# Kernel tuning notes

Hardware: AMD Instinct MI355X
Metric: run time of the kernel (lower is better)

Reference implementation:

```python
import jax, jax.numpy as jnp
import numpy as np

# model dims (see init_kwargs)
HID = 2048
H = 16
Q_LORA = 768
KV_LORA = 512
QK_NOPE = 128
QK_ROPE = 64
QK_HEAD = QK_NOPE + QK_ROPE  # 192
V_DIM = 128
HI = 8        # indexer heads
DI = 128      # indexer head dim
TOPK = 512    # index_topk
EPS = 1e-5
B, S = 1, 2048


def rms_norm(x, w):
    return x * jax.lax.rsqrt(jnp.mean(x * x, -1, keepdims=True) + EPS) * w


def layer_norm(x, w, b):
    m = jnp.mean(x, -1, keepdims=True)
    v = jnp.mean((x - m) ** 2, -1, keepdims=True)
    return (x - m) * jax.lax.rsqrt(v + EPS) * w + b


def rotate_half(x):
    x1, x2 = jnp.split(x, 2, axis=-1)
    return jnp.concatenate([-x2, x1], axis=-1)


def rope_bshd(x, cos, sin):
    # x: [B,S,H,D], cos/sin: [B,S,D] -> broadcast over heads (unsqueeze_dim=2)
    return x * cos[:, :, None, :] + rotate_half(x) * sin[:, :, None, :]


def setup_inputs() -> dict:
    key = jax.random.key(0)
    ks = jax.random.split(key, 16)
    std = 0.02
    hidden_states = jax.random.normal(ks[0], (B, S, HID), jnp.float32)
    # real RoPE tables, theta=10000, head_dim=QK_ROPE
    inv_freq = 1.0 / (10000.0 ** (np.arange(0, QK_ROPE, 2, dtype=np.float32) / QK_ROPE))
    freqs = np.arange(S, dtype=np.float32)[:, None] * inv_freq[None, :]  # [S, ROPE/2]
    emb = np.concatenate([freqs, freqs], axis=-1)
    cos = jnp.asarray(np.cos(emb))[None]  # [1,S,ROPE]
    sin = jnp.asarray(np.sin(emb))[None]
    w = lambda k, shp: jax.random.normal(k, shp, jnp.float32) * std
    return {
        'hidden_states': hidden_states, 'cos': cos, 'sin': sin,
        'wq_a': w(ks[1], (Q_LORA, HID)),
        'q_a_norm_w': jnp.ones((Q_LORA,), jnp.float32),
        'wq_b': w(ks[2], (H * QK_HEAD, Q_LORA)),
        'wkv_a': w(ks[3], (KV_LORA + QK_ROPE, HID)),
        'kv_a_norm_w': jnp.ones((KV_LORA,), jnp.float32),
        'wkv_b': w(ks[4], (H * (QK_NOPE + V_DIM), KV_LORA)),
        'wo': w(ks[5], (HID, H * V_DIM)),
        'idx_wq_b': w(ks[6], (HI * DI, Q_LORA)),
        'idx_wk': w(ks[7], (DI, HID)),
        'idx_k_norm_w': jnp.ones((DI,), jnp.float32),
        'idx_k_norm_b': jnp.zeros((DI,), jnp.float32),
        'idx_weights_w': w(ks[8], (HI, HID)),
    }


def reference(hidden_states, cos, sin, wq_a, q_a_norm_w, wq_b, wkv_a, kv_a_norm_w,
              wkv_b, wo, idx_wq_b, idx_wk, idx_k_norm_w, idx_k_norm_b, idx_weights_w):
    b, s, _ = hidden_states.shape
    # ---- MLA projections ----
    q_lora = rms_norm(hidden_states @ wq_a.T, q_a_norm_w)              # [B,S,Q_LORA]
    q = (q_lora @ wq_b.T).reshape(b, s, H, QK_HEAD)
    q_nope, q_rope = jnp.split(q, [QK_NOPE], axis=-1)
    q_rope = rope_bshd(q_rope, cos, sin)

    kv = hidden_states @ wkv_a.T                                        # [B,S,KV_LORA+ROPE]
    kv_lat, k_rope = jnp.split(kv, [KV_LORA], axis=-1)
    k_rope = k_rope * cos + rotate_half(k_rope) * sin                   # shared MQA rope key [B,S,ROPE]
    kv_lat = rms_norm(kv_lat, kv_a_norm_w)
    kvb = (kv_lat @ wkv_b.T).reshape(b, s, H, QK_NOPE + V_DIM)
    k_nope, value = jnp.split(kvb, [QK_NOPE], axis=-1)

    queries = jnp.concatenate([q_nope, q_rope], axis=-1)                # [B,S,H,QK_HEAD]
    keys = jnp.concatenate(
        [k_nope, jnp.broadcast_to(k_rope[:, :, None, :], (b, s, H, QK_ROPE))], axis=-1)

    # ---- lightning indexer (DSA): per-query top-k KV selection ----
    iq = (q_lora @ idx_wq_b.T).reshape(b, s, HI, DI)
    iq_rot, iq_pass = jnp.split(iq, [QK_ROPE], axis=-1)
    iq = jnp.concatenate([rope_bshd(iq_rot, cos, sin), iq_pass], axis=-1)
    ik = layer_norm(hidden_states @ idx_wk.T, idx_k_norm_w, idx_k_norm_b)  # [B,S,DI]
    ik_rot, ik_pass = jnp.split(ik, [QK_ROPE], axis=-1)
    ik = jnp.concatenate([ik_rot * cos + rotate_half(ik_rot) * sin, ik_pass], axis=-1)

    iscores = jnp.einsum('bqhd,bkd->bqhk', iq, ik) * (DI ** -0.5)       # [B,S,HI,S]
    iw = (hidden_states @ idx_weights_w.T) * (HI ** -0.5)               # [B,S,HI]
    iscore = jnp.einsum('bqh,bqhk->bqk', iw, iscores)                   # [B,S,S]

    causal = jnp.tril(jnp.ones((s, s), bool))
    iscore = jnp.where(causal[None], iscore, -1e9)
    _, topk_idx = jax.lax.top_k(iscore, TOPK)                           # [B,S,TOPK]
    allow = jnp.zeros((b, s, s), bool).at[
        jnp.arange(b)[:, None, None], jnp.arange(s)[None, :, None], topk_idx].set(True)
    allow = allow & causal[None]                                        # topk AND causal

    # ---- masked attention ----
    scale = QK_HEAD ** -0.5
    scores = jnp.einsum('bqhd,bkhd->bhqk', queries, keys) * scale       # [B,H,S,S]
    scores = jnp.where(allow[:, None], scores, -jnp.inf)
    probs = jax.nn.softmax(scores, axis=-1)
    out = jnp.einsum('bhqk,bkhd->bqhd', probs, value).reshape(b, s, H * V_DIM)
    return out @ wo.T
```

## Files before the change

### kernel.cpp

```cpp
#include <hip/hip_runtime.h>
#include <hip/hip_bf16.h>
#include <stdint.h>
#include <math.h>

#define S_LEN 2048
#define HIDDEN 2048
#define NHEAD 16
#define QLORA 768
#define KVLORA 512
#define QKNOPE 128
#define QKROPE 64
#define QKHEAD 192
#define VDIM 128
#define HIN 8
#define DIN 128
#define TOPKN 512
#define EPSF 1e-5f
#define DLAT 576
#define SCALE_ATT 0.07216878364870322f

typedef __bf16 bf16x8 __attribute__((ext_vector_type(8)));
typedef float  f32x4  __attribute__((ext_vector_type(4)));

static __device__ __forceinline__ float wave_reduce_sum(float v) {
    #pragma unroll
    for (int off = 32; off > 0; off >>= 1) v += __shfl_down(v, off);
    return v;
}

static __device__ __forceinline__ void splitw(__bf16* __restrict__ H,
                                              __bf16* __restrict__ L,
                                              size_t idx, float v) {
    __bf16 h = (__bf16)v;
    H[idx] = h;
    L[idx] = (__bf16)(v - (float)h);
}

static __device__ __forceinline__ void gll16(const __bf16* g, __bf16* lds_base) {
    __builtin_amdgcn_global_load_lds(
        (const __attribute__((address_space(1))) uint32_t*)g,
        (__attribute__((address_space(3))) uint32_t*)lds_base, 16, 0, 0);
}

#define PREP_BLOCKS 17280
__global__ __launch_bounds__(256) void prep_all(
        const float* __restrict__ hid,     __bf16* hidH,  __bf16* hidL,
        const float* __restrict__ wq_a,    __bf16* wqaH,  __bf16* wqaL,
        const float* __restrict__ idx_wq_b,__bf16* iwqH,  __bf16* iwqL,
        const float* __restrict__ idx_wk,  __bf16* iwkH,  __bf16* iwkL,
        const float* __restrict__ wq_b,    __bf16* wq_b_bf,
        const float* __restrict__ wkv_a,   __bf16* wkv_a_bf,
        const float* __restrict__ wkv_b,   __bf16* wkv_b_bf,
        const float* __restrict__ wo,      __bf16* wo_bf,
        __bf16* wknt) {
    int b = blockIdx.x, tid = threadIdx.x;
    const float* src; __bf16 *dH = nullptr, *dL = nullptr, *dC = nullptr;
    int base;
    if (b < 4096)        { src = hid;      dH = hidH; dL = hidL; base = b; }
    else if (b < 5632)   { src = wq_a;     dH = wqaH; dL = wqaL; base = b - 4096; }
    else if (b < 6400)   { src = idx_wq_b; dH = iwqH; dL = iwqL; base = b - 5632; }
    else if (b < 6656)   { src = idx_wk;   dH = iwkH; dL = iwkL; base = b - 6400; }
    else if (b < 8960)   { src = wq_b;     dC = wq_b_bf;  base = b - 6656; }
    else if (b < 10112)  { src = wkv_a;    dC = wkv_a_bf; base = b - 8960; }
    else if (b < 12160)  { src = wkv_b;    dC = wkv_b_bf; base = b - 10112; }
    else if (b < 16256)  { src = wo;       dC = wo_bf;    base = b - 12160; }
    else {
        int e = ((b - 16256) * 256 + tid) * 4;
        int c = e & 511, d = (e >> 9) & 127, h = e >> 16;
        f32x4 v = *(const f32x4*)(wkv_b + ((size_t)(h * 256 + d)) * 512 + c);
        #pragma unroll
        for (int j = 0; j < 4; ++j)
            wknt[(size_t)h * 65536 + (c + j) * 128 + d] = (__bf16)v[j];
        return;
    }
    int i = (base * 256 + tid) * 4;
    f32x4 v = *(const f32x4*)(src + i);
    if (dC) {
        #pragma unroll
        for (int j = 0; j < 4; ++j) dC[i + j] = (__bf16)v[j];
    } else {
        #pragma unroll
        for (int j = 0; j < 4; ++j) splitw(dH, dL, i + j, v[j]);
    }
}

#define GBM 128
#define GBN 64
#define GBK 32
template <typename OutT>
static __device__ __forceinline__ void gemm_s_core(
        const __bf16* __restrict__ A, const __bf16* __restrict__ B,
        OutT* __restrict__ C, int K, int lda, int ldb, int ldc,
        int bx, int by) {
    __shared__ __bf16 sAs[GBM * GBK];
    __shared__ __bf16 sBs[GBN * GBK];
    int tid = threadIdx.x;
    int lane = tid & 63, wid = tid >> 6;
    int quad = lane >> 4, l16 = lane & 15;
    int wm = wid >> 1, wn = wid & 1;
    int row0 = by * GBM, col0 = bx * GBN;
    int lr = lane >> 2, lk = (lane & 3) * 8;

    f32x4 acc[4][2] = {};

    for (int k0 = 0; k0 < K; k0 += GBK) {
        #pragma unroll
        for (int c = 0; c < 2; ++c) {
            int rb = (wid * 2 + c) * 16;
            gll16(A + (size_t)(row0 + rb + lr) * lda + k0 + lk, sAs + rb * GBK);
        }
        gll16(B + (size_t)(col0 + wid * 16 + lr) * ldb + k0 + lk, sBs + wid * 16 * GBK);
        __syncthreads();
        bf16x8 af[4], bfr[2];
        #pragma unroll
        for (int mi = 0; mi < 4; ++mi)
            af[mi] = *(const bf16x8*)&sAs[(wm * 64 + mi * 16 + l16) * GBK + quad * 8];
        #pragma unroll
        for (int ni = 0; ni < 2; ++ni)
            bfr[ni] = *(const bf16x8*)&sBs[(wn * 32 + ni * 16 + l16) * GBK + quad * 8];
        #pragma unroll
        for (int mi = 0; mi < 4; ++mi)
            #pragma unroll
            for (int ni = 0; ni < 2; ++ni)
                acc[mi][ni] = __builtin_amdgcn_mfma_f32_16x16x32_bf16(
                    af[mi], bfr[ni], acc[mi][ni], 0, 0, 0);
        __syncthreads();
    }
    #pragma unroll
    for (int mi = 0; mi < 4; ++mi)
        #pragma unroll
        for (int ni = 0; ni < 2; ++ni)
            #pragma unroll
            for (int r = 0; r < 4; ++r) {
                int row = row0 + wm * 64 + mi * 16 + quad * 4 + r;
                int col = col0 + wn * 32 + ni * 16 + l16;
                C[(size_t)row * ldc + col] = (OutT)acc[mi][ni][r];
            }
}

template <typename OutT>
__global__ __launch_bounds__(256) void gemm_s(const __bf16* __restrict__ A,
                                              const __bf16* __restrict__ B,
                                              OutT* __restrict__ C,
                                              int K, int lda, int ldb, int ldc,
                                              long sA, long sB, long sC) {
    gemm_s_core<OutT>(A + (size_t)blockIdx.z * sA, B + (size_t)blockIdx.z * sB,
                      C + (size_t)blockIdx.z * sC, K, lda, ldb, ldc,
                      blockIdx.x, blockIdx.y);
}

template <bool CAUSAL>
static __device__ __forceinline__ void gemm3_core(
        const __bf16* __restrict__ Ah, const __bf16* __restrict__ Al,
        const __bf16* __restrict__ Bh, const __bf16* __restrict__ Bl,
        float* __restrict__ C, int K, int lda, int ldb, int ldc,
        int row_base, int bx, int by) {
    int row0 = by * GBM + row_base, col0 = bx * GBN;
    if (CAUSAL && col0 > row0 + GBM - 1) return;
    __shared__ __bf16 sAh[GBM * GBK], sAl[GBM * GBK];
    __shared__ __bf16 sBh[GBN * GBK], sBl[GBN * GBK];
    int tid = threadIdx.x;
    int lane = tid & 63, wid = tid >> 6;
    int quad = lane >> 4, l16 = lane & 15;
    int wm = wid >> 1, wn = wid & 1;
    int lr = lane >> 2, lk = (lane & 3) * 8;

    f32x4 acc[4][2] = {};

    for (int k0 = 0; k0 < K; k0 += GBK) {
        #pragma unroll
        for (int c = 0; c < 2; ++c) {
            int rb = (wid * 2 + c) * 16;
            size_t go = (size_t)(row0 + rb + lr) * lda + k0 + lk;
            gll16(Ah + go, sAh + rb * GBK);
            gll16(Al + go, sAl + rb * GBK);
        }
        {
            size_t go = (size_t)(col0 + wid * 16 + lr) * ldb + k0 + lk;
            gll16(Bh + go, sBh + wid * 16 * GBK);
            gll16(Bl + go, sBl + wid * 16 * GBK);
        }
        __syncthreads();
        bf16x8 afh[4], afl[4], bfh[2], bfl[2];
        #pragma unroll
        for (int mi = 0; mi < 4; ++mi) {
            int o = (wm * 64 + mi * 16 + l16) * GBK + quad * 8;
            afh[mi] = *(const bf16x8*)&sAh[o];
            afl[mi] = *(const bf16x8*)&sAl[o];
        }
        #pragma unroll
        for (int ni = 0; ni < 2; ++ni) {
            int o = (wn * 32 + ni * 16 + l16) * GBK + quad * 8;
            bfh[ni] = *(const bf16x8*)&sBh[o];
            bfl[ni] = *(const bf16x8*)&sBl[o];
        }
        #pragma unroll
        for (int mi = 0; mi < 4; ++mi)
            #pragma unroll
            for (int ni = 0; ni < 2; ++ni) {
                acc[mi][ni] = __builtin_amdgcn_mfma_f32_16x16x32_bf16(
                    afl[mi], bfh[ni], acc[mi][ni], 0, 0, 0);
                acc[mi][ni] = __builtin_amdgcn_mfma_f32_16x16x32_bf16(
                    afh[mi], bfl[ni], acc[mi][ni], 0, 0, 0);
                acc[mi][ni] = __builtin_amdgcn_mfma_f32_16x16x32_bf16(
                    afh[mi], bfh[ni], acc[mi][ni], 0, 0, 0);
            }
        __syncthreads();
    }
    #pragma unroll
    for (int mi = 0; mi < 4; ++mi)
        #pragma unroll
        for (int ni = 0; ni < 2; ++ni)
            #pragma unroll
            for (int r = 0; r < 4; ++r) {
                int row = row0 + wm * 64 + mi * 16 + quad * 4 + r;
                int col = col0 + wn * 32 + ni * 16 + l16;
                C[(size_t)row * ldc + col] = acc[mi][ni][r];
            }
}

__global__ __launch_bounds__(256) void gemm3_ks(const __bf16* __restrict__ Ah,
                                                const __bf16* __restrict__ Al,
                                                const __bf16* __restrict__ Bh,
                                                const __bf16* __restrict__ Bl,
                                                float* __restrict__ Cpart,
                                                int Ksub, int lda, int ldb, int ldc,
                                                long sC) {
    int bz = blockIdx.z, koff = bz * Ksub;
    gemm3_core<false>(Ah + koff, Al + koff, Bh + koff, Bl + koff,
                      Cpart + (size_t)bz * sC, Ksub, lda, ldb, ldc, 0,
                      blockIdx.x, blockIdx.y);
}

__global__ __launch_bounds__(256) void fused_mid(
        const __bf16* __restrict__ qlH, const __bf16* __restrict__ qlL,
        const __bf16* __restrict__ wq_b_bf, __bf16* __restrict__ qbuf_bf,
        const __bf16* __restrict__ hidH, const __bf16* __restrict__ hidL,
        const __bf16* __restrict__ wkv_a_bf, float* __restrict__ kv,
        const __bf16* __restrict__ iwqH, const __bf16* __restrict__ iwqL,
        float* __restrict__ iqraw,
        const __bf16* __restrict__ iwkH, const __bf16* __restrict__ iwkL,
        float* __restrict__ ikraw) {
    int b = blockIdx.x;
    if (b < 768) {
        gemm_s_core<__bf16>(qlH, wq_b_bf, qbuf_bf, QLORA, QLORA, QLORA,
                            NHEAD * QKHEAD, b % 48, b / 48);
    } else if (b < 912) {
        int r = b - 768;
        gemm_s_core<float>(hidH, wkv_a_bf, kv, HIDDEN, HIDDEN, HIDDEN, DLAT,
                           r % 9, r / 9);
    } else if (b < 1168) {
        int r = b - 912;
        gemm3_core<false>(qlH, qlL, iwqH, iwqL, iqraw, QLORA, QLORA, QLORA,
                          HIN * DIN, 0, r & 15, r >> 4);
    } else {
        int r = b - 1168;
        gemm3_core<false>(hidH, hidL, iwkH, iwkL, ikraw, HIDDEN, HIDDEN, HIDDEN,
                          DIN, 0, r & 1, r >> 1);
    }
}

__global__ __launch_bounds__(256) void fused2(
        const __bf16* __restrict__ qbuf_bf, const __bf16* __restrict__ wknt,
        __bf16* __restrict__ qeff,
        const __bf16* __restrict__ cqH, const __bf16* __restrict__ cqL,
        const __bf16* __restrict__ ikH, const __bf16* __restrict__ ikL,
        float* __restrict__ iscore) {
    int b = blockIdx.x;
    if (b < 2048) {
        int bx = b & 7, by = (b >> 3) & 15, bz = b >> 7;
        gemm_s_core<__bf16>(qbuf_bf + bz * QKHEAD, wknt + (size_t)bz * 512 * 128,
                            qeff + bz * DLAT, 128, NHEAD * QKHEAD, 128,
                            NHEAD * DLAT, bx, by);
    } else {
        int r = b - 2048;
        gemm3_core<true>(cqH, cqL, ikH, ikL, iscore, DIN, DIN, DIN, S_LEN,
                         TOPKN, r & 31, r >> 5);
    }
}

__global__ __launch_bounds__(256) void rmsnorm_split4(const float* __restrict__ p,
                                                      long ps,
                                                      const float* __restrict__ w,
                                                      __bf16* __restrict__ yH,
                                                      __bf16* __restrict__ yL, int ncols) {
    int row = blockIdx.x, tid = threadIdx.x;
    const float* p0 = p + (size_t)row * ncols;
    float ss = 0.f;
    for (int c = tid; c < ncols; c += 256) {
        float v = p0[c] + p0[ps + c] + p0[2 * ps + c] + p0[3 * ps + c];
        ss += v * v;
    }
    __shared__ float red[4];
    ss = wave_reduce_sum(ss);
    if ((tid & 63) == 0) red[tid >> 6] = ss;
    __syncthreads();
    float tot = red[0] + red[1] + red[2] + red[3];
    float inv = rsqrtf(tot / (float)ncols + EPSF);
    for (int c = tid; c < ncols; c += 256) {
        float v = p0[c] + p0[ps + c] + p0[2 * ps + c] + p0[3 * ps + c];
        splitw(yH, yL, (size_t)row * ncols + c, v * inv * w[c]);
    }
}

__global__ __launch_bounds__(256) void fused_post(
        const __bf16* __restrict__ qbuf, __bf16* __restrict__ qeff,
        const float* __restrict__ kv, const float* __restrict__ kvw,
        __bf16* __restrict__ klat,
        const float* __restrict__ ikraw, const float* __restrict__ lnw,
        const float* __restrict__ lnb, __bf16* __restrict__ ikH, __bf16* __restrict__ ikL,
        const float* __restrict__ iqraw, const float* __restrict__ hid,
        const float* __restrict__ iww, __bf16* __restrict__ cqH, __bf16* __restrict__ cqL,
        const float* __restrict__ cosT, const float* __restrict__ sinT) {
    int s = blockIdx.x, tid = threadIdx.x;
    int lane = tid & 63, wid = tid >> 6;

    for (int i = tid; i < NHEAD * 32; i += 256) {
        int h = i >> 5, d = i & 31;
        const __bf16* base = qbuf + (size_t)s * (NHEAD * QKHEAD) + h * QKHEAD + QKNOPE;
        float x1 = (float)base[d], x2 = (float)base[d + 32];
        float c1 = cosT[s * 64 + d],      s1 = sinT[s * 64 + d];
        float c2 = cosT[s * 64 + d + 32], s2 = sinT[s * 64 + d + 32];
        __bf16* o = qeff + (size_t)s * (NHEAD * DLAT) + h * DLAT + 512;
        o[d]      = (__bf16)(x1 * c1 - x2 * s1);
        o[d + 32] = (__bf16)(x2 * c2 + x1 * s2);
    }

    {
        const float* row = kv + (size_t)s * DLAT;
        float ss = 0.f;
        for (int c = tid; c < KVLORA; c += 256) { float v = row[c]; ss += v * v; }
        __shared__ float redB[4];
        ss = wave_reduce_sum(ss);
        if (lane == 0) redB[wid] = ss;
        __syncthreads();
        float tot = redB[0] + redB[1] + redB[2] + redB[3];
        float inv = rsqrtf(tot / (float)KVLORA + EPSF);
        __bf16* orow = klat + (size_t)s * DLAT;
        for (int c = tid; c < KVLORA; c += 256)
            orow[c] = (__bf16)(row[c] * inv * kvw[c]);
        if (tid < 32) {
            int d = tid;
            float x1 = row[KVLORA + d], x2 = row[KVLORA + d + 32];
            float c1 = cosT[s * 64 + d],      s1 = sinT[s * 64 + d];
            float c2 = cosT[s * 64 + d + 32], s2 = sinT[s * 64 + d + 32];
            orow[512 + d]      = (__bf16)(x1 * c1 - x2 * s1);
            orow[512 + d + 32] = (__bf16)(x2 * c2 + x1 * s2);
        }
    }

    {
        float x = (tid < DIN) ? ikraw[(size_t)s * DIN + tid] : 0.f;
        __shared__ float redC1[4], redC2[4], sy[DIN];
        float sm = wave_reduce_sum(x);
        if (lane == 0) redC1[wid] = sm;
        __syncthreads();
        float mean = (redC1[0] + redC1[1] + redC1[2] + redC1[3]) / (float)DIN;
        float dx = (tid < DIN) ? (x - mean) : 0.f;
        float vs = wave_reduce_sum(dx * dx);
        if (lane == 0) redC2[wid] = vs;
        __syncthreads();
        float var = (redC2[0] + redC2[1] + redC2[2] + redC2[3]) / (float)DIN;
        if (tid < DIN) sy[tid] = dx * rsqrtf(var + EPSF) * lnw[tid] + lnb[tid];
        __syncthreads();
        size_t ro = (size_t)s * DIN;
        if (tid < 32) {
            int d = tid;
            float c1 = cosT[s * 64 + d],      s1 = sinT[s * 64 + d];
            float c2 = cosT[s * 64 + d + 32], s2 = sinT[s * 64 + d + 32];
            splitw(ikH, ikL, ro + d,      sy[d] * c1 - sy[d + 32] * s1);
            splitw(ikH, ikL, ro + d + 32, sy[d + 32] * c2 + sy[d] * s2);
        } else if (tid >= 64 && tid < DIN) {
            splitw(ikH, ikL, ro + tid, sy[tid]);
        }
        __syncthreads();
    }

    {
        __shared__ float redD[4][HIN], siw[HIN];
        float a8[HIN] = {};
        const float* xr = hid + (size_t)s * HIDDEN;
        for (int c = tid; c < HIDDEN; c += 256) {
            float x = xr[c];
            #pragma unroll
            for (int h = 0; h < HIN; ++h) a8[h] += x * iww[h * HIDDEN + c];
        }
        #pragma unroll
        for (int h = 0; h < HIN; ++h) a8[h] = wave_reduce_sum(a8[h]);
        if (lane == 0)
            #pragma unroll
            for (int h = 0; h < HIN; ++h) redD[wid][h] = a8[h];
        __syncthreads();
        if (tid < HIN)
            siw[tid] = redD[0][tid] + redD[1][tid] + redD[2][tid] + redD[3][tid];
        __syncthreads();
        if (tid < DIN) {
            int d = tid;
            float acc = 0.f;
            float c1 = 0.f, s1 = 0.f;
            if (d < 64) { c1 = cosT[s * 64 + d]; s1 = sinT[s * 64 + d]; }
            #pragma unroll
            for (int h = 0; h < HIN; ++h) {
                const float* base = iqraw + ((size_t)s * HIN + h) * DIN;
                float v;
                if (d < 32)       v = base[d] * c1 - base[d + 32] * s1;
                else if (d < 64)  v = base[d] * c1 + base[d - 32] * s1;
                else              v = base[d];
                acc += siw[h] * v;
            }
            splitw(cqH, cqL, (size_t)s * DIN + d, acc * 0.03125f);
        }
    }
}

__global__ __launch_bounds__(256) void topk_rows(const float* __restrict__ iscore,
                                                 int* __restrict__ topk) {
    int q = TOPKN + blockIdx.x;
    int n = q + 1;
    __shared__ uint32_t skey[S_LEN];
    __shared__ int hist[256];
    __shared__ int scan[256];
    __shared__ uint32_t sp;
    __shared__ int sr, pos;
    int tid = threadIdx.x;
    const float* row = iscore + (size_t)q * S_LEN;
    for (int i = tid; i < n; i += 256) {
        uint32_t u = __float_as_uint(row[i]);
        skey[i] = (u & 0x80000000u) ? ~u : (u | 0x80000000u);
    }
    __syncthreads();
    uint32_t prefix = 0;
    int remk = TOPKN;
    for (int pass = 0; pass < 4; ++pass) {
        int shift = 24 - 8 * pass;
        uint32_t pmask = pass ? (0xFFFFFFFFu << (shift + 8)) : 0u;
        hist[tid] = 0;
        __syncthreads();
        for (int i = tid; i < n; i += 256) {
            uint32_t u = skey[i];
            if ((u & pmask) == prefix) atomicAdd(&hist[(u >> shift) & 255], 1);
        }
        __syncthreads();
        scan[tid] = hist[tid];
        __syncthreads();
        for (int step = 1; step < 256; step <<= 1) {
            int v = (tid + step < 256) ? scan[tid + step] : 0;
            __syncthreads();
            scan[tid] += v;
            __syncthreads();
        }
        int Sb = scan[tid];
        int Snext = (tid < 255) ? scan[tid + 1] : 0;
        if (Sb >= remk && Snext < remk) {
            sp = prefix | ((uint32_t)tid << shift);
            sr = remk - Snext;
        }
        __syncthreads();
        prefix = sp; remk = sr;
        __syncthreads();
    }
    if (tid == 0) pos = 0;
    __syncthreads();
    int* orow = topk + (size_t)q * TOPKN;
    for (int i = tid; i < n; i += 256) {
        if (skey[i] > prefix) { int p = atomicAdd(&pos, 1); orow[p] = i; }
    }
    __syncthreads();
    int base = pos;
    int chunk = (n + 255) >> 8;
    int lo = tid * chunk, hiEnd = lo + chunk;
    if (hiEnd > n) hiEnd = n;
    int cnt = 0;
    for (int i = lo; i < hiEnd; ++i) cnt += (skey[i] == prefix);
    scan[tid] = cnt;
    __syncthreads();
    for (int step = 1; step < 256; step <<= 1) {
        int v = (tid >= step) ? scan[tid - step] : 0;
        __syncthreads();
        scan[tid] += v;
        __syncthreads();
    }
    int r = scan[tid] - cnt;
    for (int i = lo; i < hiEnd && r < remk; ++i) {
        if (skey[i] == prefix) { orow[base + r] = i; ++r; }
    }
}

#define SKS 584
__global__ __launch_bounds__(256) void attn2(const __bf16* __restrict__ qeff,
                                             const __bf16* __restrict__ klat,
                                             const int* __restrict__ topk,
                                             __bf16* __restrict__ o_lat) {
    int q = (blockIdx.x * 997) & (S_LEN - 1);
    int tid = threadIdx.x;
    int lane = tid & 63, wid = tid >> 6;
    int l16 = lane & 15, quad = lane >> 4;
    int wn = wid & 1, wk = wid >> 1;

    __shared__ short sK[32 * SKS];
    __shared__ float s_part[2][16][37];
    __shared__ float s_S[16][38];
    __shared__ float s_m[16], s_l[16], s_alpha[16], s_inv[16];

    int L = (q < TOPKN) ? (q + 1) : TOPKN;
    int nt = (L + 31) >> 5;
    const int* idxr = topk + (size_t)q * TOPKN;

    bf16x8 qf[9];
    const __bf16* qrow = qeff + (size_t)q * (NHEAD * DLAT) + l16 * DLAT + wk * 288 + quad * 8;
    #pragma unroll
    for (int s = 0; s < 9; ++s) qf[s] = *(const bf16x8*)(qrow + s * 32);

    if (tid < 16) { s_m[tid] = -1e30f; s_l[tid] = 0.f; }

    f32x4 oacc[8];
    #pragma unroll
    for (int i = 0; i < 8; ++i) oacc[i] = (f32x4){0.f, 0.f, 0.f, 0.f};

    int srow = tid >> 3, schk = tid & 7;

    for (int t = 0; t < nt; ++t) {
        int ki = t * 32 + srow;
        int gk = 0;
        if (ki < L) gk = (q < TOPKN) ? ki : idxr[ki];
        const uint4* src = (const uint4*)(klat + (size_t)gk * DLAT) + schk * 9;
        uint4* dst = (uint4*)((char*)sK + srow * (SKS * 2) + schk * 144);
        #pragma unroll
        for (int c = 0; c < 9; ++c) dst[c] = src[c];
        __syncthreads();

        f32x4 sacc = {0.f, 0.f, 0.f, 0.f};
        const short* kbase = sK + (wn * 16 + l16) * SKS + wk * 288 + quad * 8;
        #pragma unroll
        for (int s = 0; s < 9; ++s) {
            bf16x8 kf = *(const bf16x8*)(kbase + s * 32);
            sacc = __builtin_amdgcn_mfma_f32_16x16x32_bf16(qf[s], kf, sacc, 0, 0, 0);
        }
        #pragma unroll
        for (int r = 0; r < 4; ++r)
            s_part[wk][quad * 4 + r][wn * 16 + l16] = sacc[r];
        __syncthreads();

        {
            int h = tid >> 4, k0 = (tid & 15) * 2;
            float v0 = -1e30f, v1 = -1e30f;
            if (t * 32 + k0 < L)
                v0 = (s_part[0][h][k0] + s_part[1][h][k0]) * SCALE_ATT;
            if (t * 32 + k0 + 1 < L)
                v1 = (s_part[0][h][k0 + 1] + s_part[1][h][k0 + 1]) * SCALE_ATT;
            float mt = fmaxf(v0, v1);
            #pragma unroll
            for (int o = 1; o < 16; o <<= 1) mt = fmaxf(mt, __shfl_xor(mt, o));
            float mold = s_m[h];
            float mnew = fmaxf(mold, mt);
            float p0 = __expf(v0 - mnew), p1 = __expf(v1 - mnew);
            float ls = p0 + p1;
            #pragma unroll
            for (int o = 1; o < 16; o <<= 1) ls += __shfl_xor(ls, o);
            *(float2*)&s_S[h][k0] = make_float2(p0, p1);
            if ((tid & 15) == 0) {
                float alpha = __expf(mold - mnew);
                s_alpha[h] = alpha;
                s_m[h] = mnew;
                s_l[h] = s_l[h] * alpha + ls;
            }
        }
        __syncthreads();

        f32x4 al4 = *(const f32x4*)&s_alpha[quad * 4];
        bf16x8 pf;
        int qhi = quad & 2, qlo = quad & 1;
        #pragma unroll
        for (int p = 0; p < 4; ++p) {
            float2 v = *(const float2*)&s_S[l16][quad * 8 + ((2 * p) ^ qhi)];
            float e0 = qlo ? v.y : v.x, e1 = qlo ? v.x : v.y;
            pf[2 * p]     = (__bf16)e0;
            pf[2 * p + 1] = (__bf16)e1;
        }
        const __bf16* sKb = (const __bf16*)sK;
        #pragma unroll
        for (int n = 0; n < 8; ++n) {
            int dim = wid * 128 + n * 16 + l16;
            bf16x8 vf;
            #pragma unroll
            for (int j = 0; j < 8; ++j)
                vf[j] = sKb[(quad * 8 + (j ^ quad)) * SKS + dim];
            #pragma unroll
            for (int r = 0; r < 4; ++r) oacc[n][r] *= al4[r];
            oacc[n] = __builtin_amdgcn_mfma_f32_16x16x32_bf16(pf, vf, oacc[n], 0, 0, 0);
        }
        __syncthreads();
    }

    if (tid < 16) s_inv[tid] = 1.f / s_l[tid];
    __syncthreads();
    f32x4 inv4 = *(const f32x4*)&s_inv[quad * 4];
    #pragma unroll
    for (int n = 0; n < 8; ++n) {
        int dim = wid * 128 + n * 16 + l16;
        #pragma unroll
        for (int r = 0; r < 4; ++r) {
            int h = quad * 4 + r;
            o_lat[(size_t)q * 8192 + h * 512 + dim] = (__bf16)(oacc[n][r] * inv4[r]);
        }
    }
}

extern "C" void kernel_launch(void* const* d_in, const int* in_sizes, int n_in,
                              void* d_out, int out_size, void* d_ws, size_t ws_size,
                              hipStream_t stream) {
    const float* hid          = (const float*)d_in[0];
    const float* cosT         = (const float*)d_in[1];
    const float* sinT         = (const float*)d_in[2];
    const float* wq_a         = (const float*)d_in[3];
    const float* q_a_norm_w   = (const float*)d_in[4];
    const float* wq_b         = (const float*)d_in[5];
    const float* wkv_a        = (const float*)d_in[6];
    const float* kv_a_norm_w  = (const float*)d_in[7];
    const float* wkv_b        = (const float*)d_in[8];
    const float* wo           = (const float*)d_in[9];
    const float* idx_wq_b     = (const float*)d_in[10];
    const float* idx_wk       = (const float*)d_in[11];
    const float* idx_k_norm_w = (const float*)d_in[12];
    const float* idx_k_norm_b = (const float*)d_in[13];
    const float* idx_weights_w= (const float*)d_in[14];
    float* out = (float*)d_out;

    char* ws = (char*)d_ws;
    size_t off = 0;
    auto alloc = [&](size_t nbytes) {
        void* p = (void*)(ws + off);
        off += (nbytes + 255) & ~(size_t)255;
        return p;
    };
    __bf16* qbuf_bf  = (__bf16*)alloc((size_t)S_LEN * NHEAD * QKHEAD * 2);
    float*  kv       = (float*) alloc((size_t)S_LEN * DLAT * 4);
    __bf16* klat_bf  = (__bf16*)alloc((size_t)S_LEN * DLAT * 2);
    __bf16* qeff_bf  = (__bf16*)alloc((size_t)S_LEN * NHEAD * DLAT * 2);
    int*    topk     = (int*)   alloc((size_t)S_LEN * TOPKN * 4);
    char* uB = (char*)alloc((size_t)S_LEN * HIDDEN * 2 + (size_t)DLAT * HIDDEN * 2);
    __bf16* hidH      = (__bf16*)uB;
    __bf16* wkv_a_bf  = (__bf16*)(uB + (size_t)S_LEN * HIDDEN * 2);
    __bf16* attn_o_bf = (__bf16*)uB;
    __bf16* hidL      = (__bf16*)alloc((size_t)S_LEN * HIDDEN * 2);
    char* uC = (char*)alloc((size_t)S_LEN * NHEAD * 512 * 2);
    float*  qpart    = (float*)uC;
    __bf16* o_lat_bf = (__bf16*)uC;
    float* iqraw  = (float*)uC;
    float* ikraw  = (float*)(uC + 8388608);
    float* iscore = (float*)(uC + 11599872);
    __bf16* wq_b_bf  = (__bf16*)alloc((size_t)(NHEAD * QKHEAD) * QLORA * 2);
    __bf16* wkv_b_bf = (__bf16*)alloc((size_t)(NHEAD * 256) * KVLORA * 2);
    __bf16* wknt_bf  = (__bf16*)alloc((size_t)NHEAD * 512 * 128 * 2);
    __bf16* wo_bf    = (__bf16*)alloc((size_t)HIDDEN * (NHEAD * VDIM) * 2);
    __bf16* wqaH = (__bf16*)alloc((size_t)QLORA * HIDDEN * 2);
    __bf16* wqaL = (__bf16*)alloc((size_t)QLORA * HIDDEN * 2);
    __bf16* qlH  = (__bf16*)alloc((size_t)S_LEN * QLORA * 2);
    __bf16* qlL  = (__bf16*)alloc((size_t)S_LEN * QLORA * 2);
    __bf16* iwqH = (__bf16*)alloc((size_t)(HIN * DIN) * QLORA * 2);
    __bf16* iwqL = (__bf16*)alloc((size_t)(HIN * DIN) * QLORA * 2);
    __bf16* iwkH = (__bf16*)alloc((size_t)DIN * HIDDEN * 2);
    __bf16* iwkL = (__bf16*)alloc((size_t)DIN * HIDDEN * 2);
    __bf16* ikH  = (__bf16*)alloc((size_t)S_LEN * DIN * 2);
    __bf16* ikL  = (__bf16*)alloc((size_t)S_LEN * DIN * 2);
    __bf16* cqH  = (__bf16*)alloc((size_t)S_LEN * DIN * 2);
    __bf16* cqL  = (__bf16*)alloc((size_t)S_LEN * DIN * 2);
    (void)ws_size; (void)in_sizes; (void)n_in; (void)out_size;

    dim3 blk(256);

    prep_all<<<PREP_BLOCKS, blk, 0, stream>>>(
        hid, hidH, hidL, wq_a, wqaH, wqaL, idx_wq_b, iwqH, iwqL,
        idx_wk, iwkH, iwkL, wq_b, wq_b_bf, wkv_a, wkv_a_bf,
        wkv_b, wkv_b_bf, wo, wo_bf, wknt_bf);

    gemm3_ks<<<dim3(QLORA / GBN, S_LEN / GBM, 4), blk, 0, stream>>>(
        hidH, hidL, wqaH, wqaL, qpart, HIDDEN / 4, HIDDEN, HIDDEN, QLORA,
        (long)S_LEN * QLORA);
    rmsnorm_split4<<<S_LEN, 256, 0, stream>>>(qpart, (long)S_LEN * QLORA,
                                              q_a_norm_w, qlH, qlL, QLORA);

    fused_mid<<<1200, blk, 0, stream>>>(qlH, qlL, wq_b_bf, qbuf_bf,
                                        hidH, hidL, wkv_a_bf, kv,
                                        iwqH, iwqL, iqraw, iwkH, iwkL, ikraw);

    fused_post<<<S_LEN, 256, 0, stream>>>(qbuf_bf, qeff_bf, kv, kv_a_norm_w, klat_bf,
                                          ikraw, idx_k_norm_w, idx_k_norm_b, ikH, ikL,
                                          iqraw, hid, idx_weights_w, cqH, cqL,
                                          cosT, sinT);

    fused2<<<2048 + 384, blk, 0, stream>>>(qbuf_bf, wknt_bf, qeff_bf,
                                           cqH, cqL, ikH, ikL, iscore);

    topk_rows<<<S_LEN - TOPKN, 256, 0, stream>>>(iscore, topk);

    attn2<<<S_LEN, 256, 0, stream>>>(qeff_bf, klat_bf, topk, o_lat_bf);

    gemm_s<__bf16><<<dim3(VDIM / GBN, S_LEN / GBM, NHEAD), blk, 0, stream>>>(
        o_lat_bf, wkv_b_bf + 128 * 512, attn_o_bf, 512,
        NHEAD * 512, 512, NHEAD * VDIM, 512, 256 * 512, VDIM);
    gemm_s<float><<<dim3(HIDDEN / GBN, S_LEN / GBM, 1), blk, 0, stream>>>(
        attn_o_bf, wo_bf, out, NHEAD * VDIM,
        NHEAD * VDIM, NHEAD * VDIM, HIDDEN, 0, 0, 0);
}
```

Baseline: 559.0 us.

## Overlap top-k selection with causal-prefix attention rows and speed up scans

Merges the top-k kernel with attention for the first 512 query rows, which need no top-k indices, into one launch so the two run concurrently on different blocks through a shared-memory union. The remaining 1536 rows run attention in a separate launch. The top-k scans switch from barrier-heavy shared-memory Hillis-Steele loops to wave-shuffle scans, and the K tile load uses gll16 direct-to-LDS loads. The risks are larger shared-memory use for the top-k blocks, which may lower occupancy, and an extra launch.

```diff
diff --git a/kernel.cpp b/kernel.cpp
--- a/kernel.cpp
+++ b/kernel.cpp
@@ -413,95 +413,118 @@
     }
 }
 
-__global__ __launch_bounds__(256) void topk_rows(const float* __restrict__ iscore,
-                                                 int* __restrict__ topk) {
-    int q = TOPKN + blockIdx.x;
+#define SKS 584
+struct AttnSmem {
+    short sK[32 * SKS];
+    float s_part[2][16][37];
+    float s_S[16][38];
+    float s_m[16], s_l[16], s_alpha[16], s_inv[16];
+};
+struct TopkSmem {
+    uint32_t skey[S_LEN];
+    int hist[256];
+    int wtot[4];
+    uint32_t sp;
+    int sr;
+    int pos;
+};
+
+static __device__ __forceinline__ int suffix_scan256(int v, int tid, int* wtot) {
+    int lane = tid & 63, w = tid >> 6;
+    #pragma unroll
+    for (int off = 1; off < 64; off <<= 1) {
+        int u = __shfl_down(v, off);
+        v += (lane + off < 64) ? u : 0;
+    }
+    int wt = __shfl(v, 0);
+    if (lane == 0) wtot[w] = wt;
+    __syncthreads();
+    int add = 0;
+    #pragma unroll
+    for (int w2 = 0; w2 < 4; ++w2) add += (w2 > w) ? wtot[w2] : 0;
+    return v + add;
+}
+
+static __device__ __forceinline__ int prefix_scan256_excl(int v, int tid, int* wtot) {
+    int lane = tid & 63, w = tid >> 6;
+    int orig = v;
+    #pragma unroll
+    for (int off = 1; off < 64; off <<= 1) {
+        int u = __shfl_up(v, off);
+        v += (lane >= off) ? u : 0;
+    }
+    int wt = __shfl(v, 63);
+    if (lane == 0) wtot[w] = wt;
+    __syncthreads();
+    int add = 0;
+    #pragma unroll
+    for (int w2 = 0; w2 < 4; ++w2) add += (w2 < w) ? wtot[w2] : 0;
+    return v + add - orig;
+}
+
+static __device__ void topk_body(TopkSmem& sm, int qi,
+                                 const float* __restrict__ iscore,
+                                 int* __restrict__ topk) {
+    int q = TOPKN + qi;
     int n = q + 1;
-    __shared__ uint32_t skey[S_LEN];
-    __shared__ int hist[256];
-    __shared__ int scan[256];
-    __shared__ uint32_t sp;
-    __shared__ int sr, pos;
     int tid = threadIdx.x;
     const float* row = iscore + (size_t)q * S_LEN;
     for (int i = tid; i < n; i += 256) {
         uint32_t u = __float_as_uint(row[i]);
-        skey[i] = (u & 0x80000000u) ? ~u : (u | 0x80000000u);
-    }
-    __syncthreads();
+        sm.skey[i] = (u & 0x80000000u) ? ~u : (u | 0x80000000u);
+    }
     uint32_t prefix = 0;
     int remk = TOPKN;
     for (int pass = 0; pass < 4; ++pass) {
         int shift = 24 - 8 * pass;
         uint32_t pmask = pass ? (0xFFFFFFFFu << (shift + 8)) : 0u;
-        hist[tid] = 0;
+        sm.hist[tid] = 0;
         __syncthreads();
         for (int i = tid; i < n; i += 256) {
-            uint32_t u = skey[i];
-            if ((u & pmask) == prefix) atomicAdd(&hist[(u >> shift) & 255], 1);
-        }
-        __syncthreads();
-        scan[tid] = hist[tid];
-        __syncthreads();
-        for (int step = 1; step < 256; step <<= 1) {
-            int v = (tid + step < 256) ? scan[tid + step] : 0;
-            __syncthreads();
-            scan[tid] += v;
-            __syncthreads();
-        }
-        int Sb = scan[tid];
-        int Snext = (tid < 255) ? scan[tid + 1] : 0;
+            uint32_t u = sm.skey[i];
+            if ((u & pmask) == prefix) atomicAdd(&sm.hist[(u >> shift) & 255], 1);
+        }
+        __syncthreads();
+        int cnt = sm.hist[tid];
+        int Sb = suffix_scan256(cnt, tid, sm.wtot);
+        int Snext = Sb - cnt;
         if (Sb >= remk && Snext < remk) {
-            sp = prefix | ((uint32_t)tid << shift);
-            sr = remk - Snext;
-        }
-        __syncthreads();
-        prefix = sp; remk = sr;
-        __syncthreads();
-    }
-    if (tid == 0) pos = 0;
+            sm.sp = prefix | ((uint32_t)tid << shift);
+            sm.sr = remk - Snext;
+        }
+        __syncthreads();
+        prefix = sm.sp;
+        remk = sm.sr;
+    }
+    if (tid == 0) sm.pos = 0;
     __syncthreads();
     int* orow = topk + (size_t)q * TOPKN;
     for (int i = tid; i < n; i += 256) {
-        if (skey[i] > prefix) { int p = atomicAdd(&pos, 1); orow[p] = i; }
+        if (sm.skey[i] > prefix) { int p = atomicAdd(&sm.pos, 1); orow[p] = i; }
     }
     __syncthreads();
-    int base = pos;
+    int base = sm.pos;
     int chunk = (n + 255) >> 8;
     int lo = tid * chunk, hiEnd = lo + chunk;
     if (hiEnd > n) hiEnd = n;
     int cnt = 0;
-    for (int i = lo; i < hiEnd; ++i) cnt += (skey[i] == prefix);
-    scan[tid] = cnt;
-    __syncthreads();
-    for (int step = 1; step < 256; step <<= 1) {
-        int v = (tid >= step) ? scan[tid - step] : 0;
-        __syncthreads();
-        scan[tid] += v;
-        __syncthreads();
-    }
-    int r = scan[tid] - cnt;
+    for (int i = lo; i < hiEnd; ++i) cnt += (sm.skey[i] == prefix);
+    int r = prefix_scan256_excl(cnt, tid, sm.wtot);
     for (int i = lo; i < hiEnd && r < remk; ++i) {
-        if (skey[i] == prefix) { orow[base + r] = i; ++r; }
-    }
-}
-
-#define SKS 584
-__global__ __launch_bounds__(256) void attn2(const __bf16* __restrict__ qeff,
-                                             const __bf16* __restrict__ klat,
-                                             const int* __restrict__ topk,
-                                             __bf16* __restrict__ o_lat) {
-    int q = (blockIdx.x * 997) & (S_LEN - 1);
+        if (sm.skey[i] == prefix) { orow[base + r] = i; ++r; }
+    }
+}
+
+static __device__ void attn_body(AttnSmem& sm, int q,
+                                 const __bf16* __restrict__ qeff,
+                                 const __bf16* __restrict__ klat,
+                                 const int* __restrict__ topk,
+                                 __bf16* __restrict__ o_lat) {
     int tid = threadIdx.x;
     int lane = tid & 63, wid = tid >> 6;
     int l16 = lane & 15, quad = lane >> 4;
     int wn = wid & 1, wk = wid >> 1;
 
-    __shared__ short sK[32 * SKS];
-    __shared__ float s_part[2][16][37];
-    __shared__ float s_S[16][38];
-    __shared__ float s_m[16], s_l[16], s_alpha[16], s_inv[16];
-
     int L = (q < TOPKN) ? (q + 1) : TOPKN;
     int nt = (L + 31) >> 5;
     const int* idxr = topk + (size_t)q * TOPKN;
@@ -511,26 +534,29 @@
     #pragma unroll
     for (int s = 0; s < 9; ++s) qf[s] = *(const bf16x8*)(qrow + s * 32);
 
-    if (tid < 16) { s_m[tid] = -1e30f; s_l[tid] = 0.f; }
+    if (tid < 16) { sm.s_m[tid] = -1e30f; sm.s_l[tid] = 0.f; }
 
     f32x4 oacc[8];
     #pragma unroll
     for (int i = 0; i < 8; ++i) oacc[i] = (f32x4){0.f, 0.f, 0.f, 0.f};
 
-    int srow = tid >> 3, schk = tid & 7;
-
     for (int t = 0; t < nt; ++t) {
-        int ki = t * 32 + srow;
-        int gk = 0;
-        if (ki < L) gk = (q < TOPKN) ? ki : idxr[ki];
-        const uint4* src = (const uint4*)(klat + (size_t)gk * DLAT) + schk * 9;
-        uint4* dst = (uint4*)((char*)sK + srow * (SKS * 2) + schk * 144);
-        #pragma unroll
-        for (int c = 0; c < 9; ++c) dst[c] = src[c];
+        #pragma unroll
+        for (int i = 0; i < 8; ++i) {
+            int row = wid * 8 + i;
+            int ki = t * 32 + row;
+            int gk = 0;
+            if (ki < L) gk = (q < TOPKN) ? ki : idxr[ki];
+            const __bf16* src = klat + (size_t)gk * DLAT;
+            gll16(src + lane * 8, (__bf16*)&sm.sK[row * SKS]);
+            if (lane < 8)
+                *(uint4*)&sm.sK[row * SKS + 512 + lane * 8] =
+                    *(const uint4*)(src + 512 + lane * 8);
+        }
         __syncthreads();
 
         f32x4 sacc = {0.f, 0.f, 0.f, 0.f};
-        const short* kbase = sK + (wn * 16 + l16) * SKS + wk * 288 + quad * 8;
+        const short* kbase = sm.sK + (wn * 16 + l16) * SKS + wk * 288 + quad * 8;
         #pragma unroll
         for (int s = 0; s < 9; ++s) {
             bf16x8 kf = *(const bf16x8*)(kbase + s * 32);
@@ -538,46 +564,46 @@
         }
         #pragma unroll
         for (int r = 0; r < 4; ++r)
-            s_part[wk][quad * 4 + r][wn * 16 + l16] = sacc[r];
+            sm.s_part[wk][quad * 4 + r][wn * 16 + l16] = sacc[r];
         __syncthreads();
 
         {
             int h = tid >> 4, k0 = (tid & 15) * 2;
             float v0 = -1e30f, v1 = -1e30f;
             if (t * 32 + k0 < L)
-                v0 = (s_part[0][h][k0] + s_part[1][h][k0]) * SCALE_ATT;
+                v0 = (sm.s_part[0][h][k0] + sm.s_part[1][h][k0]) * SCALE_ATT;
             if (t * 32 + k0 + 1 < L)
-                v1 = (s_part[0][h][k0 + 1] + s_part[1][h][k0 + 1]) * SCALE_ATT;
+                v1 = (sm.s_part[0][h][k0 + 1] + sm.s_part[1][h][k0 + 1]) * SCALE_ATT;
             float mt = fmaxf(v0, v1);
             #pragma unroll
             for (int o = 1; o < 16; o <<= 1) mt = fmaxf(mt, __shfl_xor(mt, o));
-            float mold = s_m[h];
+            float mold = sm.s_m[h];
             float mnew = fmaxf(mold, mt);
             float p0 = __expf(v0 - mnew), p1 = __expf(v1 - mnew);
             float ls = p0 + p1;
             #pragma unroll
             for (int o = 1; o < 16; o <<= 1) ls += __shfl_xor(ls, o);
-            *(float2*)&s_S[h][k0] = make_float2(p0, p1);
+            *(float2*)&sm.s_S[h][k0] = make_float2(p0, p1);
             if ((tid & 15) == 0) {
                 float alpha = __expf(mold - mnew);
-                s_alpha[h] = alpha;
-                s_m[h] = mnew;
-                s_l[h] = s_l[h] * alpha + ls;
+                sm.s_alpha[h] = alpha;
+                sm.s_m[h] = mnew;
+                sm.s_l[h] = sm.s_l[h] * alpha + ls;
             }
         }
         __syncthreads();
 
-        f32x4 al4 = *(const f32x4*)&s_alpha[quad * 4];
+        f32x4 al4 = *(const f32x4*)&sm.s_alpha[quad * 4];
         bf16x8 pf;
         int qhi = quad & 2, qlo = quad & 1;
         #pragma unroll
         for (int p = 0; p < 4; ++p) {
-            float2 v = *(const float2*)&s_S[l16][quad * 8 + ((2 * p) ^ qhi)];
+            float2 v = *(const float2*)&sm.s_S[l16][quad * 8 + ((2 * p) ^ qhi)];
             float e0 = qlo ? v.y : v.x, e1 = qlo ? v.x : v.y;
             pf[2 * p]     = (__bf16)e0;
             pf[2 * p + 1] = (__bf16)e1;
         }
-        const __bf16* sKb = (const __bf16*)sK;
+        const __bf16* sKb = (const __bf16*)sm.sK;
         #pragma unroll
         for (int n = 0; n < 8; ++n) {
             int dim = wid * 128 + n * 16 + l16;
@@ -592,9 +618,9 @@
         __syncthreads();
     }
 
-    if (tid < 16) s_inv[tid] = 1.f / s_l[tid];
+    if (tid < 16) sm.s_inv[tid] = 1.f / sm.s_l[tid];
     __syncthreads();
-    f32x4 inv4 = *(const f32x4*)&s_inv[quad * 4];
+    f32x4 inv4 = *(const f32x4*)&sm.s_inv[quad * 4];
     #pragma unroll
     for (int n = 0; n < 8; ++n) {
         int dim = wid * 128 + n * 16 + l16;
@@ -604,6 +630,28 @@
             o_lat[(size_t)q * 8192 + h * 512 + dim] = (__bf16)(oacc[n][r] * inv4[r]);
         }
     }
+}
+
+__global__ __launch_bounds__(256) void topk_attnA(
+        const float* __restrict__ iscore, int* __restrict__ topk,
+        const __bf16* __restrict__ qeff, const __bf16* __restrict__ klat,
+        __bf16* __restrict__ o_lat) {
+    __shared__ __align__(16) char pool[sizeof(AttnSmem)];
+    int b = blockIdx.x;
+    if (b < 512) {
+        attn_body(*(AttnSmem*)pool, (b * 997) & 511, qeff, klat, nullptr, o_lat);
+    } else {
+        topk_body(*(TopkSmem*)pool, b - 512, iscore, topk);
+    }
+}
+
+__global__ __launch_bounds__(256) void attn2b(const __bf16* __restrict__ qeff,
+                                              const __bf16* __restrict__ klat,
+                                              const int* __restrict__ topk,
+                                              __bf16* __restrict__ o_lat) {
+    __shared__ __align__(16) char pool[sizeof(AttnSmem)];
+    int q = TOPKN + (blockIdx.x * 997) % (S_LEN - TOPKN);
+    attn_body(*(AttnSmem*)pool, q, qeff, klat, topk, o_lat);
 }
 
 extern "C" void kernel_launch(void* const* d_in, const int* in_sizes, int n_in,
@@ -692,9 +740,9 @@
     fused2<<<2048 + 384, blk, 0, stream>>>(qbuf_bf, wknt_bf, qeff_bf,
                                            cqH, cqL, ikH, ikL, iscore);
 
-    topk_rows<<<S_LEN - TOPKN, 256, 0, stream>>>(iscore, topk);
-
-    attn2<<<S_LEN, 256, 0, stream>>>(qeff_bf, klat_bf, topk, o_lat_bf);
+    topk_attnA<<<512 + 1536, blk, 0, stream>>>(iscore, topk, qeff_bf, klat_bf, o_lat_bf);
+
+    attn2b<<<S_LEN - TOPKN, blk, 0, stream>>>(qeff_bf, klat_bf, topk, o_lat_bf);
 
     gemm_s<__bf16><<<dim3(VDIM / GBN, S_LEN / GBM, NHEAD), blk, 0, stream>>>(
         o_lat_bf, wkv_b_bf + 128 * 512, attn_o_bf, 512,
```

After: 979.8 us. +75.3%, slower.
